# Optimization experiments

Measured on AMD Instinct MI355X. Metric: run time of the kernel, lower is better.

## Reference

```python
import jax, jax.numpy as jnp
import numpy as np

ANGSTROM_TO_METER = 1e-10
COULOMB_CONSTANT = 8987551792.3
ELECTRON_CHARGE = 1.602176634e-19
EV_TO_JOULE = 1.602176634e-19
COUL_DAMPING_BETA = 18.7
R0_METER = 2.2 * ANGSTROM_TO_METER
EWALD_P = 0.3275911
EWALD_A = (0.254829592, -0.284496736, 1.421413741, -1.453152027, 1.061405429)
EWALD_F = 2.0

N_ATOMS = 200000
N_EDGES = 8000000
N_GRAPHS = 256


def setup_inputs() -> dict:
    key = jax.random.key(0)
    k1, k2, k3, k4, k5 = jax.random.split(key, 5)
    dij = jax.random.normal(k1, (N_EDGES, 3), dtype=jnp.float32)  # Angstrom
    pred_charge = jax.random.normal(k2, (N_ATOMS,), dtype=jnp.float32)  # e
    g_ewald = jnp.full((1,), 3.0e9, dtype=jnp.float32)  # 1/m (~0.3 1/A)
    row = jax.random.randint(k3, (N_EDGES,), 0, N_ATOMS)
    col = jax.random.randint(k4, (N_EDGES,), 0, N_ATOMS)
    batch = jnp.sort(jax.random.randint(k5, (N_ATOMS,), 0, N_GRAPHS))
    return {"dij": dij, "pred_charge": pred_charge, "g_ewald": g_ewald,
            "row": row, "col": col, "batch": batch}


def reference(dij, pred_charge, g_ewald, row, col, batch):
    n_atoms = pred_charge.shape[0]
    dij_m = dij * ANGSTROM_TO_METER                      # [E,3] meters
    rij = jnp.sqrt(jnp.sum(dij_m * dij_m, axis=-1))      # [E]
    q = pred_charge * ELECTRON_CHARGE                    # Coulombs
    prefactor = COULOMB_CONSTANT * q[row] * q[col] / rij
    # exponential short-range damping below r0
    damp = jnp.where(rij < R0_METER,
                     jnp.exp(-COUL_DAMPING_BETA * (R0_METER - rij) / R0_METER),
                     jnp.ones_like(rij))
    ecoul = 0.5 * prefactor * damp
    fcoul = prefactor * damp / rij
    # Ewald real-space correction via Abramowitz-Stegun erfc polynomial
    grij = g_ewald[0] * rij
    expm2 = jnp.exp(-grij * grij)
    t = 1.0 / (1.0 + EWALD_P * grij)
    a0, a1, a2, a3, a4 = EWALD_A
    erfc = t * (a0 + t * (a1 + t * (a2 + t * (a3 + t * a4)))) * expm2
    ecoul = ecoul + prefactor * (erfc - 1.0)
    fcoul = fcoul + prefactor * (erfc + EWALD_F * grij * expm2 - 1.0) / rij
    # per-edge force vector, converted J/m -> eV/A
    fij = dij_m * (fcoul / rij)[:, None]                 # [E,3]
    fij_ev = fij * ANGSTROM_TO_METER / EV_TO_JOULE
    ecoul_ev = ecoul / EV_TO_JOULE
    # scatter edge->atom (by row), then atom->molecule (by batch)
    e_atom = jax.ops.segment_sum(ecoul_ev, row, num_segments=n_atoms)
    coul_energy = jax.ops.segment_sum(e_atom, batch, num_segments=N_GRAPHS)
    force_row = jax.ops.segment_sum(fij_ev, row, num_segments=n_atoms)
    force_col = jax.ops.segment_sum(fij_ev, col, num_segments=n_atoms)
    coul_force = force_row - force_col
    return coul_energy, coul_force
```

## Files before the change

### kernel.cpp

```cpp
#include <hip/hip_runtime.h>
#include <hip/hip_fp16.h>

#define N_GRAPHS_C 256
#define CHUNK_LOG 12
#define CHUNK (1 << CHUNK_LOG)
#define MAXB 64
#define NSLICE 12
#define NSLICE_FB 10
#define TPA 256
#define TPBB 1024
#define SD 64
#define SSTR (2 * SD + 1)
#define PSTR (CHUNK + 8)
#define FP_SCALE 1024.0f
#define FP_INV   (1.0f / 1024.0f)

__device__ __forceinline__ void edge_math(
    float dx, float dy, float dz, float qr, float qc, float gA,
    float& fx, float& fy, float& fz, float& ecoul)
{
    const float KEV = (float)(8987551792.3 * 1.602176634e-9);
    float r2 = dx * dx + dy * dy + dz * dz;
    float inv_r = rsqrtf(r2);
    float rA = r2 * inv_r;

    float pref = KEV * qr * qc * inv_r;

    float damp = 1.0f;
    if (rA < 2.2f)
        damp = __expf(-18.7f * (2.2f - rA) * (1.0f / 2.2f));

    float grij = gA * rA;
    float expm2 = __expf(-grij * grij);
    float t = 1.0f / (1.0f + 0.3275911f * grij);
    float erfc = t * (0.254829592f +
                 t * (-0.284496736f +
                 t * (1.421413741f +
                 t * (-1.453152027f +
                 t * 1.061405429f)))) * expm2;

    ecoul = pref * (0.5f * damp + (erfc - 1.0f));
    float S = damp + erfc + 2.0f * grij * expm2 - 1.0f;
    float fs = pref * S * (inv_r * inv_r);
    fx = dx * fs; fy = dy * fs; fz = dz * fs;
}

__device__ __forceinline__ uint2 pack_rec(float fx, float fy, float fz, unsigned lid)
{
    uint2 u;
    u.x = __builtin_bit_cast(unsigned, __floats2half2_rn(fx, fy));
    u.y = (__builtin_bit_cast(unsigned, __floats2half2_rn(fz, 0.0f)) & 0xFFFFu) |
          (lid << 16);
    return u;
}

__device__ __forceinline__ void acc_rec(int* acc, unsigned w0, unsigned w1)
{
    float2 xy = __half22float2(__builtin_bit_cast(__half2, w0));
    float fz = __half2float(__builtin_bit_cast(__half2, w1).x);
    unsigned idx = w1 >> 16;
    atomicAdd(&acc[idx],            __float2int_rn(xy.x * FP_SCALE));
    atomicAdd(&acc[PSTR + idx],     __float2int_rn(xy.y * FP_SCALE));
    atomicAdd(&acc[2 * PSTR + idx], __float2int_rn(fz   * FP_SCALE));
}

__global__ __launch_bounds__(256) void prep_qg(
    const float* __restrict__ q, const int* __restrict__ batch,
    float2* __restrict__ qg, float* __restrict__ ovf, int* __restrict__ fint,
    int n_atoms)
{
    int i = blockIdx.x * 256 + threadIdx.x;
    if (i < n_atoms) {
        qg[i] = make_float2(q[i], __int_as_float(batch[i]));
        ovf[3 * i + 0] = 0.f;
        ovf[3 * i + 1] = 0.f;
        ovf[3 * i + 2] = 0.f;
        fint[i] = 0;
        fint[n_atoms + i] = 0;
        fint[2 * n_atoms + i] = 0;
    }
}

__global__ __launch_bounds__(TPA) void passA(
    const float* __restrict__ dij, const float2* __restrict__ qg,
    const float* __restrict__ g_ewald,
    const int* __restrict__ row, const int* __restrict__ col,
    uint2* __restrict__ records, int cap,
    unsigned* __restrict__ cnt_table,
    float* __restrict__ e_part,
    float* __restrict__ ovf,
    int n_edges, int nb, int tile_g)
{
    __shared__ unsigned stageU[MAXB * SSTR];
    __shared__ unsigned scnt[MAXB];
    __shared__ unsigned cnt[MAXB];
    __shared__ float    e_graph[4 * N_GRAPHS_C];

    int tid  = threadIdx.x;
    int wid  = tid >> 6;
    int lane = tid & 63;
    if (tid < MAXB) { scnt[tid] = 0u; cnt[tid] = 0u; }
    for (int i = tid; i < 4 * N_GRAPHS_C; i += TPA) e_graph[i] = 0.f;
    __syncthreads();

    float* e_my = &e_graph[wid * N_GRAPHS_C];

    int n4 = n_edges >> 2;
    int gbase = blockIdx.x * tile_g;
    int g1 = min(gbase + tile_g, n4);
    int nph = tile_g / TPA;

    const int4* row4 = (const int4*)row;
    const int4* col4 = (const int4*)col;
    const float4* dij4 = (const float4*)dij;

    const float gA = g_ewald[0] * 1e-10f;
    size_t blk_base = (size_t)blockIdx.x * nb * cap;

    int4 r_cur = make_int4(0, 0, 0, 0), c_cur = make_int4(0, 0, 0, 0);
    float2 vr_cur[4], vc_cur[4];
    {
        int g = gbase + tid;
        if (g < g1) { r_cur = row4[g]; c_cur = col4[g]; }
        vr_cur[0] = qg[r_cur.x]; vc_cur[0] = qg[c_cur.x];
        vr_cur[1] = qg[r_cur.y]; vc_cur[1] = qg[c_cur.y];
        vr_cur[2] = qg[r_cur.z]; vc_cur[2] = qg[c_cur.z];
        vr_cur[3] = qg[r_cur.w]; vc_cur[3] = qg[c_cur.w];
    }

    for (int p = 0; p < nph; ++p) {
        int g = gbase + p * TPA + tid;

        int4 r_nxt = make_int4(0, 0, 0, 0), c_nxt = make_int4(0, 0, 0, 0);
        if (p + 1 < nph && g + TPA < g1) {
            r_nxt = row4[g + TPA]; c_nxt = col4[g + TPA];
        }

        if (g < g1) {
            float4 d0 = dij4[3 * g + 0];
            float4 d1 = dij4[3 * g + 1];
            float4 d2 = dij4[3 * g + 2];
            float ex[4] = {d0.x, d0.w, d1.z, d2.y};
            float ey[4] = {d0.y, d1.x, d1.w, d2.z};
            float ez[4] = {d0.z, d1.y, d2.x, d2.w};
            int rr[4] = {r_cur.x, r_cur.y, r_cur.z, r_cur.w};
            int cc[4] = {c_cur.x, c_cur.y, c_cur.z, c_cur.w};

            #pragma unroll
            for (int j = 0; j < 4; ++j) {
                int r = rr[j], c = cc[j];
                float fx, fy, fz, ec;
                edge_math(ex[j], ey[j], ez[j], vr_cur[j].x, vc_cur[j].x, gA,
                          fx, fy, fz, ec);

                atomicAdd(&e_my[__float_as_int(vr_cur[j].y)], ec);

                int br = r >> CHUNK_LOG, bc = c >> CHUNK_LOG;
                unsigned pr = atomicAdd(&scnt[br], 1u);
                unsigned pc = atomicAdd(&scnt[bc], 1u);
                if (pr < SD) {
                    uint2 rv = pack_rec(fx, fy, fz, (unsigned)(r & (CHUNK - 1)));
                    int bi = br * SSTR + 2 * (int)pr;
                    stageU[bi] = rv.x; stageU[bi + 1] = rv.y;
                } else {
                    atomicAdd(&ovf[3 * r + 0], fx);
                    atomicAdd(&ovf[3 * r + 1], fy);
                    atomicAdd(&ovf[3 * r + 2], fz);
                }
                if (pc < SD) {
                    uint2 rv = pack_rec(-fx, -fy, -fz, (unsigned)(c & (CHUNK - 1)));
                    int bi = bc * SSTR + 2 * (int)pc;
                    stageU[bi] = rv.x; stageU[bi + 1] = rv.y;
                } else {
                    atomicAdd(&ovf[3 * c + 0], -fx);
                    atomicAdd(&ovf[3 * c + 1], -fy);
                    atomicAdd(&ovf[3 * c + 2], -fz);
                }
            }
        }

        float2 vr_n[4], vc_n[4];
        vr_n[0] = qg[r_nxt.x]; vc_n[0] = qg[c_nxt.x];
        vr_n[1] = qg[r_nxt.y]; vc_n[1] = qg[c_nxt.y];
        vr_n[2] = qg[r_nxt.z]; vc_n[2] = qg[c_nxt.z];
        vr_n[3] = qg[r_nxt.w]; vc_n[3] = qg[c_nxt.w];

        __syncthreads();

        for (int b = wid; b < nb; b += TPA / 64) {
            unsigned m = min(scnt[b], (unsigned)SD);
            unsigned base = 0;
            if (lane == 0) base = atomicAdd(&cnt[b], m);
            base = (unsigned)__shfl((int)base, 0, 64);
            int sb = b * SSTR;
            for (unsigned i = lane; i < m; i += 64) {
                uint2 rv = make_uint2(stageU[sb + 2 * i], stageU[sb + 2 * i + 1]);
                unsigned slot = base + i;
                if (slot < (unsigned)cap) {
                    records[blk_base + (size_t)b * cap + slot] = rv;
                } else {
                    float2 xy = __half22float2(__builtin_bit_cast(__half2, rv.x));
                    float fzv = __half2float(__builtin_bit_cast(__half2, rv.y).x);
                    int atom = (b << CHUNK_LOG) + (int)(rv.y >> 16);
                    atomicAdd(&ovf[3 * atom + 0], xy.x);
                    atomicAdd(&ovf[3 * atom + 1], xy.y);
                    atomicAdd(&ovf[3 * atom + 2], fzv);
                }
            }
            if (lane == 0) scnt[b] = 0u;
        }
        __syncthreads();

        r_cur = r_nxt; c_cur = c_nxt;
        #pragma unroll
        for (int j = 0; j < 4; ++j) { vr_cur[j] = vr_n[j]; vc_cur[j] = vc_n[j]; }
    }

    if (tid < nb) cnt_table[(size_t)blockIdx.x * nb + tid] = min(cnt[tid], (unsigned)cap);
    for (int g2 = tid; g2 < N_GRAPHS_C; g2 += TPA)
        e_part[(size_t)blockIdx.x * N_GRAPHS_C + g2] =
            e_graph[g2] + e_graph[N_GRAPHS_C + g2] +
            e_graph[2 * N_GRAPHS_C + g2] + e_graph[3 * N_GRAPHS_C + g2];
}

__global__ __launch_bounds__(TPBB) void passB(
    const uint2* __restrict__ records, int cap,
    const unsigned* __restrict__ cnt_table,
    int* __restrict__ fint, int nblkA, int nb, int nslice, int n_atoms)
{
    __shared__ int acc[3 * PSTR];

    int b = blockIdx.x / nslice;
    int s = blockIdx.x % nslice;
    int k0 = (int)((long long)s * nblkA / nslice);
    int k1 = (int)((long long)(s + 1) * nblkA / nslice);

    for (int i = threadIdx.x; i < 3 * PSTR; i += TPBB) acc[i] = 0;
    __syncthreads();

    int wid  = threadIdx.x >> 6;
    int lane = threadIdx.x & 63;
    const int W = TPBB / 64;

    for (int kb = k0 + wid; kb < k1; kb += 4 * W) {
        int ka = kb, kB = kb + W, kc = kb + 2 * W, kd = kb + 3 * W;
        bool e1 = kB < k1, e2 = kc < k1, e3 = kd < k1;

        unsigned n0 = cnt_table[(size_t)ka * nb + b];
        unsigned n1 = e1 ? cnt_table[(size_t)kB * nb + b] : 0u;
        unsigned n2 = e2 ? cnt_table[(size_t)kc * nb + b] : 0u;
        unsigned n3 = e3 ? cnt_table[(size_t)kd * nb + b] : 0u;

        const uint2* r0 = records + ((size_t)ka * nb + b) * cap;
        const uint2* r1 = e1 ? records + ((size_t)kB * nb + b) * cap : r0;
        const uint2* r2 = e2 ? records + ((size_t)kc * nb + b) * cap : r0;
        const uint2* r3 = e3 ? records + ((size_t)kd * nb + b) * cap : r0;
        const uint4* q0 = (const uint4*)r0;
        const uint4* q1 = (const uint4*)r1;
        const uint4* q2 = (const uint4*)r2;
        const uint4* q3 = (const uint4*)r3;

        unsigned h0 = n0 >> 1, h1 = n1 >> 1, h2 = n2 >> 1, h3 = n3 >> 1;
        unsigned hm = max(max(h0, h1), max(h2, h3));

        for (unsigned i = lane; i < hm; i += 64) {
            uint4 v0 = q0[h0 ? min(i, h0 - 1u) : 0u];
            uint4 v1 = q1[h1 ? min(i, h1 - 1u) : 0u];
            uint4 v2 = q2[h2 ? min(i, h2 - 1u) : 0u];
            uint4 v3 = q3[h3 ? min(i, h3 - 1u) : 0u];
            if (i < h0) { acc_rec(acc, v0.x, v0.y); acc_rec(acc, v0.z, v0.w); }
            if (i < h1) { acc_rec(acc, v1.x, v1.y); acc_rec(acc, v1.z, v1.w); }
            if (i < h2) { acc_rec(acc, v2.x, v2.y); acc_rec(acc, v2.z, v2.w); }
            if (i < h3) { acc_rec(acc, v3.x, v3.y); acc_rec(acc, v3.z, v3.w); }
        }
        if (lane == 0) {
            if (n0 & 1u) { uint2 t = r0[n0 - 1]; acc_rec(acc, t.x, t.y); }
            if (n1 & 1u) { uint2 t = r1[n1 - 1]; acc_rec(acc, t.x, t.y); }
            if (n2 & 1u) { uint2 t = r2[n2 - 1]; acc_rec(acc, t.x, t.y); }
            if (n3 & 1u) { uint2 t = r3[n3 - 1]; acc_rec(acc, t.x, t.y); }
        }
    }
    __syncthreads();

    int abase = b << CHUNK_LOG;
    for (int i = threadIdx.x; i < 3 * CHUNK; i += TPBB) {
        int pl  = i >> CHUNK_LOG;
        int ofs = i & (CHUNK - 1);
        int v = acc[pl * PSTR + ofs];
        int a = abase + ofs;
        if (v != 0 && a < n_atoms)
            atomicAdd(&fint[pl * n_atoms + a], v);
    }
}

__global__ __launch_bounds__(256) void fin_force(
    const int* __restrict__ fint, const float* __restrict__ ovf,
    const float* __restrict__ e_part,
    float* __restrict__ force, float* __restrict__ energy,
    int n_atoms, int nblkA, int nfblk)
{
    if ((int)blockIdx.x >= nfblk) {
        int g = (blockIdx.x - nfblk) * 4 + (threadIdx.x >> 6);
        int lane = threadIdx.x & 63;
        float s = 0.f;
        for (int k = lane; k < nblkA; k += 64)
            s += e_part[(size_t)k * N_GRAPHS_C + g];
        for (int off = 32; off > 0; off >>= 1) s += __shfl_down(s, off, 64);
        if (lane == 0) energy[g] = s;
        return;
    }
    int a = blockIdx.x * 256 + threadIdx.x;
    if (a >= n_atoms) return;
    force[3 * a + 0] = ovf[3 * a + 0] + (float)fint[a] * FP_INV;
    force[3 * a + 1] = ovf[3 * a + 1] + (float)fint[n_atoms + a] * FP_INV;
    force[3 * a + 2] = ovf[3 * a + 2] + (float)fint[2 * n_atoms + a] * FP_INV;
}

__global__ __launch_bounds__(1024) void chunk_kernel(
    const float* __restrict__ dij, const float* __restrict__ q,
    const float* __restrict__ g_ewald,
    const int* __restrict__ row, const int* __restrict__ col,
    float* __restrict__ partial, int n_edges, int n_chunks, int n_slices)
{
    __shared__ float acc[CHUNK * 4];
    int c = blockIdx.x % n_chunks;
    int p = blockIdx.x / n_chunks;
    int cbase = c << CHUNK_LOG;
    for (int i = threadIdx.x; i < CHUNK * 4; i += 1024) acc[i] = 0.f;
    __syncthreads();
    const float gA = g_ewald[0] * 1e-10f;
    int n4 = (n_edges + 3) >> 2;
    int g0 = (int)((long long)p * n4 / n_slices);
    int g1 = (int)((long long)(p + 1) * n4 / n_slices);
    const int4* row4 = (const int4*)row;
    const int4* col4 = (const int4*)col;
    for (int g = g0 + threadIdx.x; g < g1; g += 1024) {
        int4 r4 = row4[g];
        int4 c4 = col4[g];
        int rr[4] = {r4.x, r4.y, r4.z, r4.w};
        int cc[4] = {c4.x, c4.y, c4.z, c4.w};
        #pragma unroll
        for (int j = 0; j < 4; ++j) {
            int e = 4 * g + j;
            if (e >= n_edges) break;
            int rl = rr[j] - cbase;
            int cl = cc[j] - cbase;
            bool hr = (unsigned)rl < (unsigned)CHUNK;
            bool hc = (unsigned)cl < (unsigned)CHUNK;
            if (!(hr || hc)) continue;
            float fx, fy, fz, ec;
            edge_math(dij[3 * e], dij[3 * e + 1], dij[3 * e + 2],
                      q[rr[j]], q[cc[j]], gA, fx, fy, fz, ec);
            if (hr) {
                atomicAdd(&acc[4 * rl + 0], fx);
                atomicAdd(&acc[4 * rl + 1], fy);
                atomicAdd(&acc[4 * rl + 2], fz);
                atomicAdd(&acc[4 * rl + 3], ec);
            }
            if (hc) {
                atomicAdd(&acc[4 * cl + 0], -fx);
                atomicAdd(&acc[4 * cl + 1], -fy);
                atomicAdd(&acc[4 * cl + 2], -fz);
            }
        }
    }
    __syncthreads();
    float4* dst = (float4*)partial + (size_t)(c * n_slices + p) * CHUNK;
    const float4* src = (const float4*)acc;
    for (int i = threadIdx.x; i < CHUNK; i += 1024) dst[i] = src[i];
}

__global__ __launch_bounds__(256) void finalize_kernel(
    const float* __restrict__ partial, const int* __restrict__ batch,
    float* __restrict__ energy, float* __restrict__ force,
    int n_atoms, int n_slices)
{
    int i = blockIdx.x * blockDim.x + threadIdx.x;
    float fx = 0.f, fy = 0.f, fz = 0.f, en = 0.f;
    if (i < n_atoms) {
        int c = i >> CHUNK_LOG;
        int l = i & (CHUNK - 1);
        const float4* base = (const float4*)partial + (size_t)c * n_slices * CHUNK + l;
        for (int p = 0; p < n_slices; ++p) {
            float4 v = base[(size_t)p * CHUNK];
            fx += v.x; fy += v.y; fz += v.z; en += v.w;
        }
        force[3 * i + 0] = fx;
        force[3 * i + 1] = fy;
        force[3 * i + 2] = fz;
    }
    int ic = i < n_atoms ? i : (n_atoms - 1);
    int b = batch[ic];
    float v = (i < n_atoms) ? en : 0.0f;
    int b0 = __shfl(b, 0, 64);
    unsigned long long m = __ballot(b == b0);
    if (m == ~0ull) {
        for (int off = 32; off > 0; off >>= 1)
            v += __shfl_down(v, off, 64);
        if ((threadIdx.x & 63) == 0) atomicAdd(&energy[b0], v);
    } else {
        atomicAdd(&energy[b], v);
    }
}

extern "C" void kernel_launch(void* const* d_in, const int* in_sizes, int n_in,
                              void* d_out, int out_size, void* d_ws, size_t ws_size,
                              hipStream_t stream) {
    const float* dij     = (const float*)d_in[0];
    const float* q       = (const float*)d_in[1];
    const float* g_ewald = (const float*)d_in[2];
    const int*   row     = (const int*)d_in[3];
    const int*   col     = (const int*)d_in[4];
    const int*   batch   = (const int*)d_in[5];

    int n_edges = in_sizes[0] / 3;
    int n_atoms = in_sizes[1];

    float* energy = (float*)d_out;
    float* force  = (float*)d_out + N_GRAPHS_C;

    int nb = (n_atoms + CHUNK - 1) >> CHUNK_LOG;
    int n4 = n_edges >> 2;

    size_t sz_fint    = (size_t)3 * n_atoms * sizeof(int);
    size_t sz_ovf     = (size_t)3 * n_atoms * sizeof(float);
    size_t sz_qg      = (size_t)n_atoms * sizeof(float2);

    const int  tile_sel[2]   = {1024, 2048};
    const int  mincap_sel[2] = {224, 416};
    const int  capmax_sel[2] = {256, 512};

    int tile_g = 0, cap = 0, nblkA = 0;
    size_t sz_epart = 0, sz_cnt = 0;
    for (int t = 0; t < 2 && tile_g == 0; ++t) {
        int nba = (n4 + tile_sel[t] - 1) / tile_sel[t];
        size_t se = (size_t)nba * N_GRAPHS_C * sizeof(float);
        size_t sc = (size_t)nba * nb * sizeof(unsigned);
        size_t fixed = ((sz_fint + 255) & ~(size_t)255) +
                       ((se      + 255) & ~(size_t)255) +
                       ((sc      + 255) & ~(size_t)255) +
                       ((sz_ovf  + 255) & ~(size_t)255) +
                       ((sz_qg   + 255) & ~(size_t)255) + 512;
        if ((long long)ws_size > (long long)fixed) {
            long long c = ((long long)ws_size - (long long)fixed) /
                          ((long long)nba * nb * 8);
            c = (c / 32) * 32;
            if (c > capmax_sel[t]) c = capmax_sel[t];
            if (c >= mincap_sel[t]) {
                tile_g = tile_sel[t]; cap = (int)c; nblkA = nba;
                sz_epart = se; sz_cnt = sc;
            }
        }
    }

    bool fast = (nb <= MAXB) && ((n_edges & 3) == 0) && (tile_g > 0) &&
                ((tile_g % TPA) == 0);

    if (fast) {
        char* ws = (char*)d_ws;
        size_t off = 0;
        uint2*    records  = (uint2*)(ws + off);
        off += (size_t)nblkA * nb * cap * 8;   off = (off + 255) & ~(size_t)255;
        int*      fint     = (int*)(ws + off);
        off += sz_fint;                        off = (off + 255) & ~(size_t)255;
        float*    e_part   = (float*)(ws + off);
        off += sz_epart;                       off = (off + 255) & ~(size_t)255;
        unsigned* cnt_tab  = (unsigned*)(ws + off);
        off += sz_cnt;                         off = (off + 255) & ~(size_t)255;
        float*    ovf      = (float*)(ws + off);
        off += sz_ovf;                         off = (off + 255) & ~(size_t)255;
        float2*   qg       = (float2*)(ws + off);

        prep_qg<<<(n_atoms + 255) / 256, 256, 0, stream>>>(
            q, batch, qg, ovf, fint, n_atoms);

        passA<<<nblkA, TPA, 0, stream>>>(
            dij, qg, g_ewald, row, col,
            records, cap, cnt_tab, e_part, ovf, n_edges, nb, tile_g);

        passB<<<nb * NSLICE, TPBB, 0, stream>>>(
            records, cap, cnt_tab, fint, nblkA, nb, NSLICE, n_atoms);

        int nfblk = (n_atoms + 255) / 256;
        fin_force<<<nfblk + N_GRAPHS_C / 4, 256, 0, stream>>>(
            fint, ovf, e_part, force, energy, n_atoms, nblkA, nfblk);
    } else {
        size_t need_chunk = (size_t)nb * NSLICE_FB * CHUNK * 4 * sizeof(float);
        if (ws_size >= need_chunk) {
            hipMemsetAsync(d_out, 0, N_GRAPHS_C * sizeof(float), stream);
            chunk_kernel<<<nb * NSLICE_FB, 1024, 0, stream>>>(
                dij, q, g_ewald, row, col, (float*)d_ws, n_edges, nb, NSLICE_FB);
            finalize_kernel<<<(n_atoms + 255) / 256, 256, 0, stream>>>(
                (const float*)d_ws, batch, energy, force, n_atoms, NSLICE_FB);
        }
    }
}
```

Baseline: 347.0 us.

## Transpose record buffers to bucket-major and parallelize per-graph energy reduction

Records and count table are reindexed bucket-major (bucket, passA block) so each passB wave reads four consecutive passA blocks' contiguous records. The load clamping is replaced with predicated loads. The energy reduction in fin_force now uses coalesced per-thread column sums over NEB slices combined with atomicAdd, with energy zeroed in prep_qg. The goal is better memory locality in passB and a less serial energy reduction, at the cost of nondeterministic float atomic ordering for energy.

```diff
diff --git a/kernel.cpp b/kernel.cpp
--- a/kernel.cpp
+++ b/kernel.cpp
@@ -12,6 +12,7 @@
 #define SD 64
 #define SSTR (2 * SD + 1)
 #define PSTR (CHUNK + 8)
+#define NEB 16
 #define FP_SCALE 1024.0f
 #define FP_INV   (1.0f / 1024.0f)
 
@@ -67,7 +68,7 @@
 __global__ __launch_bounds__(256) void prep_qg(
     const float* __restrict__ q, const int* __restrict__ batch,
     float2* __restrict__ qg, float* __restrict__ ovf, int* __restrict__ fint,
-    int n_atoms)
+    float* __restrict__ energy, int n_atoms)
 {
     int i = blockIdx.x * 256 + threadIdx.x;
     if (i < n_atoms) {
@@ -79,6 +80,7 @@
         fint[n_atoms + i] = 0;
         fint[2 * n_atoms + i] = 0;
     }
+    if (i < N_GRAPHS_C) energy[i] = 0.f;
 }
 
 __global__ __launch_bounds__(TPA) void passA(
@@ -115,7 +117,6 @@
     const float4* dij4 = (const float4*)dij;
 
     const float gA = g_ewald[0] * 1e-10f;
-    size_t blk_base = (size_t)blockIdx.x * nb * cap;
 
     int4 r_cur = make_int4(0, 0, 0, 0), c_cur = make_int4(0, 0, 0, 0);
     float2 vr_cur[4], vc_cur[4];
@@ -193,11 +194,12 @@
             if (lane == 0) base = atomicAdd(&cnt[b], m);
             base = (unsigned)__shfl((int)base, 0, 64);
             int sb = b * SSTR;
+            size_t rbase = ((size_t)b * gridDim.x + blockIdx.x) * cap;
             for (unsigned i = lane; i < m; i += 64) {
                 uint2 rv = make_uint2(stageU[sb + 2 * i], stageU[sb + 2 * i + 1]);
                 unsigned slot = base + i;
                 if (slot < (unsigned)cap) {
-                    records[blk_base + (size_t)b * cap + slot] = rv;
+                    records[rbase + slot] = rv;
                 } else {
                     float2 xy = __half22float2(__builtin_bit_cast(__half2, rv.x));
                     float fzv = __half2float(__builtin_bit_cast(__half2, rv.y).x);
@@ -216,7 +218,9 @@
         for (int j = 0; j < 4; ++j) { vr_cur[j] = vr_n[j]; vc_cur[j] = vc_n[j]; }
     }
 
-    if (tid < nb) cnt_table[(size_t)blockIdx.x * nb + tid] = min(cnt[tid], (unsigned)cap);
+    if (tid < nb)
+        cnt_table[(size_t)tid * gridDim.x + blockIdx.x] =
+            min(cnt[tid], (unsigned)cap);
     for (int g2 = tid; g2 < N_GRAPHS_C; g2 += TPA)
         e_part[(size_t)blockIdx.x * N_GRAPHS_C + g2] =
             e_graph[g2] + e_graph[N_GRAPHS_C + g2] +
@@ -242,38 +246,43 @@
     int lane = threadIdx.x & 63;
     const int W = TPBB / 64;
 
-    for (int kb = k0 + wid; kb < k1; kb += 4 * W) {
-        int ka = kb, kB = kb + W, kc = kb + 2 * W, kd = kb + 3 * W;
+    const unsigned* ct = cnt_table + (size_t)b * nblkA;
+    const uint2* rb = records + (size_t)b * nblkA * cap;
+
+    for (int kb = k0 + 4 * wid; kb < k1; kb += 4 * W) {
+        int ka = kb, kB = kb + 1, kc = kb + 2, kd = kb + 3;
         bool e1 = kB < k1, e2 = kc < k1, e3 = kd < k1;
 
-        unsigned n0 = cnt_table[(size_t)ka * nb + b];
-        unsigned n1 = e1 ? cnt_table[(size_t)kB * nb + b] : 0u;
-        unsigned n2 = e2 ? cnt_table[(size_t)kc * nb + b] : 0u;
-        unsigned n3 = e3 ? cnt_table[(size_t)kd * nb + b] : 0u;
-
-        const uint2* r0 = records + ((size_t)ka * nb + b) * cap;
-        const uint2* r1 = e1 ? records + ((size_t)kB * nb + b) * cap : r0;
-        const uint2* r2 = e2 ? records + ((size_t)kc * nb + b) * cap : r0;
-        const uint2* r3 = e3 ? records + ((size_t)kd * nb + b) * cap : r0;
-        const uint4* q0 = (const uint4*)r0;
-        const uint4* q1 = (const uint4*)r1;
-        const uint4* q2 = (const uint4*)r2;
-        const uint4* q3 = (const uint4*)r3;
+        unsigned n0 = ct[ka];
+        unsigned n1 = e1 ? ct[kB] : 0u;
+        unsigned n2 = e2 ? ct[kc] : 0u;
+        unsigned n3 = e3 ? ct[kd] : 0u;
+
+        const uint4* q0 = (const uint4*)(rb + (size_t)ka * cap);
+        const uint4* q1 = (const uint4*)(rb + (size_t)kB * cap);
+        const uint4* q2 = (const uint4*)(rb + (size_t)kc * cap);
+        const uint4* q3 = (const uint4*)(rb + (size_t)kd * cap);
 
         unsigned h0 = n0 >> 1, h1 = n1 >> 1, h2 = n2 >> 1, h3 = n3 >> 1;
         unsigned hm = max(max(h0, h1), max(h2, h3));
 
         for (unsigned i = lane; i < hm; i += 64) {
-            uint4 v0 = q0[h0 ? min(i, h0 - 1u) : 0u];
-            uint4 v1 = q1[h1 ? min(i, h1 - 1u) : 0u];
-            uint4 v2 = q2[h2 ? min(i, h2 - 1u) : 0u];
-            uint4 v3 = q3[h3 ? min(i, h3 - 1u) : 0u];
-            if (i < h0) { acc_rec(acc, v0.x, v0.y); acc_rec(acc, v0.z, v0.w); }
-            if (i < h1) { acc_rec(acc, v1.x, v1.y); acc_rec(acc, v1.z, v1.w); }
-            if (i < h2) { acc_rec(acc, v2.x, v2.y); acc_rec(acc, v2.z, v2.w); }
-            if (i < h3) { acc_rec(acc, v3.x, v3.y); acc_rec(acc, v3.z, v3.w); }
+            bool a0 = i < h0, a1 = i < h1, a2 = i < h2, a3 = i < h3;
+            uint4 v0, v1, v2, v3;
+            if (a0) v0 = q0[i];
+            if (a1) v1 = q1[i];
+            if (a2) v2 = q2[i];
+            if (a3) v3 = q3[i];
+            if (a0) { acc_rec(acc, v0.x, v0.y); acc_rec(acc, v0.z, v0.w); }
+            if (a1) { acc_rec(acc, v1.x, v1.y); acc_rec(acc, v1.z, v1.w); }
+            if (a2) { acc_rec(acc, v2.x, v2.y); acc_rec(acc, v2.z, v2.w); }
+            if (a3) { acc_rec(acc, v3.x, v3.y); acc_rec(acc, v3.z, v3.w); }
         }
         if (lane == 0) {
+            const uint2* r0 = rb + (size_t)ka * cap;
+            const uint2* r1 = rb + (size_t)kB * cap;
+            const uint2* r2 = rb + (size_t)kc * cap;
+            const uint2* r3 = rb + (size_t)kd * cap;
             if (n0 & 1u) { uint2 t = r0[n0 - 1]; acc_rec(acc, t.x, t.y); }
             if (n1 & 1u) { uint2 t = r1[n1 - 1]; acc_rec(acc, t.x, t.y); }
             if (n2 & 1u) { uint2 t = r2[n2 - 1]; acc_rec(acc, t.x, t.y); }
@@ -300,13 +309,14 @@
     int n_atoms, int nblkA, int nfblk)
 {
     if ((int)blockIdx.x >= nfblk) {
-        int g = (blockIdx.x - nfblk) * 4 + (threadIdx.x >> 6);
-        int lane = threadIdx.x & 63;
+        int bi = blockIdx.x - nfblk;
+        int g  = threadIdx.x;
+        int k0 = (int)((long long)bi * nblkA / NEB);
+        int k1 = (int)((long long)(bi + 1) * nblkA / NEB);
         float s = 0.f;
-        for (int k = lane; k < nblkA; k += 64)
+        for (int k = k0; k < k1; ++k)
             s += e_part[(size_t)k * N_GRAPHS_C + g];
-        for (int off = 32; off > 0; off >>= 1) s += __shfl_down(s, off, 64);
-        if (lane == 0) energy[g] = s;
+        atomicAdd(&energy[g], s);
         return;
     }
     int a = blockIdx.x * 256 + threadIdx.x;
@@ -472,7 +482,7 @@
         float2*   qg       = (float2*)(ws + off);
 
         prep_qg<<<(n_atoms + 255) / 256, 256, 0, stream>>>(
-            q, batch, qg, ovf, fint, n_atoms);
+            q, batch, qg, ovf, fint, energy, n_atoms);
 
         passA<<<nblkA, TPA, 0, stream>>>(
             dij, qg, g_ewald, row, col,
@@ -482,7 +492,7 @@
             records, cap, cnt_tab, fint, nblkA, nb, NSLICE, n_atoms);
 
         int nfblk = (n_atoms + 255) / 256;
-        fin_force<<<nfblk + N_GRAPHS_C / 4, 256, 0, stream>>>(
+        fin_force<<<nfblk + NEB, 256, 0, stream>>>(
             fint, ovf, e_part, force, energy, n_atoms, nblkA, nfblk);
     } else {
         size_t need_chunk = (size_t)nb * NSLICE_FB * CHUNK * 4 * sizeof(float);
```

After: 380.8 us. 1.1x slower.
